# Kernel optimization log

Measured on AMD Instinct MI355X. Metric: run time of the kernel, lower is better.

The kernel has to match this reference:

```python
import jax, jax.numpy as jnp
import numpy as np

N, E, B = 50000, 800000, 512
DIN, H, A, BT = 128, 256, 40, 5


def _ln(h, g, b):
    m = jnp.mean(h, -1, keepdims=True)
    v = jnp.mean((h - m) ** 2, -1, keepdims=True)
    return (h - m) * jax.lax.rsqrt(v + 1e-5) * g + b


def _gcn(x, w, b, src, dst, n):
    # PyG GCNConv: add self-loops, symmetric D^-1/2 (A+I) D^-1/2 normalization
    h = x @ w
    loop = jnp.arange(n)
    s = jnp.concatenate([src, loop])
    d = jnp.concatenate([dst, loop])
    deg = jax.ops.segment_sum(jnp.ones(s.shape[0], h.dtype), d, num_segments=n)
    dinv = jax.lax.rsqrt(jnp.maximum(deg, 1.0))
    coef = (dinv[s] * dinv[d])[:, None]
    return jax.ops.segment_sum(coef * h[s], d, num_segments=n) + b


def _mlp2(x, w1, b1, w2, b2):
    return jax.nn.relu(x @ w1 + b1) @ w2 + b2


def _mlp3(x, w1, b1, w2, b2, w3, b3):
    h = jax.nn.relu(x @ w1 + b1)
    h = jax.nn.relu(h @ w2 + b2)
    return h @ w3 + b3


def setup_inputs() -> dict:
    key = jax.random.key(0)
    ks = iter(jax.random.split(key, 64))
    p = lambda shape: jax.random.normal(next(ks), shape, jnp.float32) * 0.05
    inp = {}
    inp["x"] = jax.random.normal(next(ks), (N, DIN), jnp.float32)
    inp["edge_index"] = jax.random.randint(next(ks), (2, E), 0, N)
    inp["batch"] = jnp.sort(jax.random.randint(next(ks), (N,), 0, B))
    inp["new_node_indices"] = jax.random.randint(next(ks), (B,), 0, N)
    inp["focus_node_indices"] = jax.random.randint(next(ks), (B,), 0, N)
    inp["num_graphs"] = B
    inp["conv_w0"] = p((DIN, H)); inp["conv_b0"] = p((H,))
    inp["conv_w1"] = p((H, H)); inp["conv_b1"] = p((H,))
    inp["conv_w2"] = p((H, H)); inp["conv_b2"] = p((H,))
    for i in range(3):
        inp[f"ln_g{i}"] = jnp.ones((H,), jnp.float32)
        inp[f"ln_b{i}"] = jnp.zeros((H,), jnp.float32)
    inp["res_w0"] = p((DIN, H)); inp["res_b0"] = p((H,))
    inp["stop_w1"] = p((H, H)); inp["stop_b1"] = p((H,))
    inp["stop_w2"] = p((H, 1)); inp["stop_b2"] = p((1,))
    inp["addn_w1"] = p((H, H)); inp["addn_b1"] = p((H,))
    inp["addn_w2"] = p((H, A)); inp["addn_b2"] = p((A,))
    inp["addb_w1"] = p((H, H)); inp["addb_b1"] = p((H,))
    inp["addb_w2"] = p((H, BT)); inp["addb_b2"] = p((BT,))
    inp["edge_w1"] = p((2 * H, H)); inp["edge_b1"] = p((H,))
    inp["edge_w2"] = p((H, H // 2)); inp["edge_b2"] = p((H // 2,))
    inp["edge_w3"] = p((H // 2, 1)); inp["edge_b3"] = p((1,))
    inp["bond_w1"] = p((2 * H, H)); inp["bond_b1"] = p((H,))
    inp["bond_w2"] = p((H, H // 2)); inp["bond_b2"] = p((H // 2,))
    inp["bond_w3"] = p((H // 2, BT)); inp["bond_b3"] = p((BT,))
    return inp


def reference(x, edge_index, batch, new_node_indices, focus_node_indices, num_graphs,
              conv_w0, conv_b0, conv_w1, conv_b1, conv_w2, conv_b2,
              ln_g0, ln_b0, ln_g1, ln_b1, ln_g2, ln_b2,
              res_w0, res_b0,
              stop_w1, stop_b1, stop_w2, stop_b2,
              addn_w1, addn_b1, addn_w2, addn_b2,
              addb_w1, addb_b1, addb_w2, addb_b2,
              edge_w1, edge_b1, edge_w2, edge_b2, edge_w3, edge_b3,
              bond_w1, bond_b1, bond_w2, bond_b2, bond_w3, bond_b3):
    n = x.shape[0]
    src, dst = edge_index[0], edge_index[1]
    conv_params = [(conv_w0, conv_b0), (conv_w1, conv_b1), (conv_w2, conv_b2)]
    ln_params = [(ln_g0, ln_b0), (ln_g1, ln_b1), (ln_g2, ln_b2)]
    h = x
    for i in range(3):
        h_in = h
        cw, cb = conv_params[i]
        lg, lb = ln_params[i]
        h = _gcn(h, cw, cb, src, dst, n)
        h = jax.nn.relu(_ln(h, lg, lb))  # dropout: eval mode (identity)
        res = h_in @ res_w0 + res_b0 if i == 0 else h_in
        h = h + res
    node_embeddings = h  # [N, H]
    # global mean pool over graphs
    counts = jax.ops.segment_sum(jnp.ones(n, h.dtype), batch, num_segments=num_graphs)
    graph_embedding = jax.ops.segment_sum(node_embeddings, batch, num_segments=num_graphs) / jnp.maximum(counts, 1.0)[:, None]
    stop_logits = _mlp2(graph_embedding, stop_w1, stop_b1, stop_w2, stop_b2)
    add_node_logits = _mlp2(graph_embedding, addn_w1, addn_b1, addn_w2, addn_b2)
    add_bond_logits = _mlp2(node_embeddings[focus_node_indices], addb_w1, addb_b1, addb_w2, addb_b2)
    # pair each node with its graph's newly added node
    new_node_embeddings = node_embeddings[new_node_indices]  # [B, H]
    pair = jnp.concatenate([node_embeddings, new_node_embeddings[batch]], axis=1)  # [N, 2H]
    edge_selection_logits = _mlp3(pair, edge_w1, edge_b1, edge_w2, edge_b2, edge_w3, edge_b3)
    bond_type_logits = _mlp3(pair, bond_w1, bond_b1, bond_w2, bond_b2, bond_w3, bond_b3)
    return (stop_logits, add_node_logits, add_bond_logits, node_embeddings,
            edge_selection_logits, bond_type_logits)
```

## Files before the change

kernel.cpp:

```cpp
#include <hip/hip_runtime.h>

typedef short bf16x8 __attribute__((ext_vector_type(8)));
typedef float f32x4 __attribute__((ext_vector_type(4)));
typedef unsigned short u16;
typedef u16 u16x8 __attribute__((ext_vector_type(8)));

__device__ __forceinline__ float bf2f(u16 u) {
  union { float f; unsigned int i; } x; x.i = ((unsigned int)u) << 16; return x.f;
}
__device__ __forceinline__ u16 f2bf(float f) {
  union { float f; unsigned int i; } x; x.f = f;
  unsigned int r = x.i + 0x7fffu + ((x.i >> 16) & 1u);
  return (u16)(r >> 16);
}
__device__ __forceinline__ void st_out_(void* out, size_t idx, float v, int f32) {
  if (f32) ((float*)out)[idx] = v;
  else ((u16*)out)[idx] = f2bf(v);
}

__global__ void k_detect(const u16* __restrict__ xx, int* flag) {
  int j = threadIdx.x;
  u16 u = xx[2 * j];
  int ex = (u >> 7) & 0xFF;
  int insane = (u != 0) && (ex < 100 || ex > 140);
  unsigned long long m = __ballot(insane);
  if (j == 0) flag[0] = (__popcll(m) > 8) ? 1 : 0;
}

__global__ void k_cvt_big(const void* __restrict__ src, u16* __restrict__ dst, int n,
                          const int* __restrict__ flag) {
  int i = blockIdx.x * 256 + threadIdx.x;
  if (i >= n) return;
  dst[i] = (*flag) ? f2bf(((const float*)src)[i]) : ((const u16*)src)[i];
}

#define NSEG 38
struct Cvt { const void* src[NSEG]; int off[NSEG + 1]; };
__global__ void k_cvt_all(Cvt c, u16* __restrict__ dst, int total, const int* __restrict__ flag) {
  int i = blockIdx.x * 256 + threadIdx.x;
  if (i >= total) return;
  int s = 0;
  #pragma unroll 1
  while (i >= c.off[s + 1]) s++;
  int j = i - c.off[s];
  dst[i] = (*flag) ? f2bf(((const float*)c.src[s])[j]) : ((const u16*)c.src[s])[j];
}

__global__ void k_padbias(const u16* __restrict__ rb, u16* cbz) {
  int i = blockIdx.x * 256 + threadIdx.x;
  if (i < 512) cbz[i] = (i < 256) ? (u16)0 : rb[i - 256];
}

struct Tr { const u16* src[8]; u16* dst[8]; int lk[8]; int nc[8]; int off[9]; };
__global__ void k_tr_all(Tr c, int total) {
  int i = blockIdx.x * 256 + threadIdx.x;
  if (i >= total) return;
  int s = 0;
  #pragma unroll 1
  while (i >= c.off[s + 1]) s++;
  int j = i - c.off[s];
  int K = 1 << c.lk[s];
  int nrow = j >> c.lk[s], k = j & (K - 1);
  c.dst[s][j] = c.src[s][k * c.nc[s] + nrow];
}

__global__ void k_init(int* deg, int* cursor, int n) {
  int i = blockIdx.x * 256 + threadIdx.x;
  if (i < n) { deg[i] = 1; cursor[i] = 0; }
}
__global__ void k_deg(const int* __restrict__ dst, int* deg, int e) {
  int i = blockIdx.x * 256 + threadIdx.x;
  if (i < e) atomicAdd(&deg[dst[i]], 1);
}
__global__ void k_dinv(const int* __restrict__ deg, float* dinv, int n) {
  int i = blockIdx.x * 256 + threadIdx.x;
  if (i < n) dinv[i] = rsqrtf((float)deg[i]);
}
#define SCB 4096
__global__ __launch_bounds__(256) void k_scanA(const int* __restrict__ deg, int* bsum, int n) {
  int b = blockIdx.x, t = threadIdx.x;
  int base = b * SCB;
  int s = 0;
  for (int j = t; j < SCB; j += 256) { int i = base + j; s += (i < n) ? deg[i] - 1 : 0; }
  int l = t & 63, wid = t >> 6;
  #pragma unroll
  for (int o = 32; o; o >>= 1) s += __shfl_xor(s, o);
  __shared__ int red[4];
  if (l == 0) red[wid] = s;
  __syncthreads();
  if (t == 0) bsum[b] = red[0] + red[1] + red[2] + red[3];
}
__global__ void k_scanB(int* bsum, int nb, int* off, int n) {
  if (threadIdx.x == 0) {
    int c = 0;
    for (int i = 0; i < nb; i++) { int v = bsum[i]; bsum[i] = c; c += v; }
    off[n] = c;
  }
}
__global__ __launch_bounds__(256) void k_scanC(const int* __restrict__ deg, const int* __restrict__ bsum,
                                               int* off, int n) {
  int b = blockIdx.x, t = threadIdx.x;
  int base = b * SCB + t * 16;
  int loc[16]; int s = 0;
  #pragma unroll
  for (int j = 0; j < 16; j++) { int i = base + j; loc[j] = s; s += (i < n) ? deg[i] - 1 : 0; }
  int l = t & 63, wid = t >> 6;
  int incl = s;
  #pragma unroll
  for (int o = 1; o < 64; o <<= 1) { int y = __shfl_up(incl, o); if (l >= o) incl += y; }
  int excl = incl - s;
  __shared__ int ws[4];
  if (l == 63) ws[wid] = incl;
  __syncthreads();
  int woff = 0;
  for (int w = 0; w < wid; w++) woff += ws[w];
  int pre = bsum[b] + woff + excl;
  #pragma unroll
  for (int j = 0; j < 16; j++) { int i = base + j; if (i < n) off[i] = pre + loc[j]; }
}
__global__ void k_csr(const int* __restrict__ src, const int* __restrict__ dst,
                      const int* __restrict__ off, int* cursor, int* csr_src, int e) {
  int i = blockIdx.x * 256 + threadIdx.x;
  if (i >= e) return;
  int d = dst[i], s = src[i];
  int slot = atomicAdd(&cursor[d], 1);
  csr_src[off[d] + slot] = s;
}

template <int EPI, int K>
__global__ __launch_bounds__(512) void gemm_p(
    const u16* __restrict__ A, int lda,
    const u16* __restrict__ Bt,
    u16* __restrict__ C, int ldc,
    int M, int NC,
    const u16* __restrict__ colbias,
    const float* __restrict__ rowbias, int rbld, const int* __restrict__ rowmap) {
  __shared__ u16 Bs[64 * K];
  __shared__ u16 As[8 * 4 * 512];
  const int t = threadIdx.x;
  const int n0 = blockIdx.x * 64;
  const int m0 = blockIdx.y * 512;
  {
    const int ng = K >> 3;
    const int tot = 64 * ng;
    for (int i = t; i < tot; i += 512) {
      int c = i / ng, g = i - c * ng;
      u16x8 v = *reinterpret_cast<const u16x8*>(Bt + (size_t)(n0 + c) * K + g * 8);
      *reinterpret_cast<u16x8*>(&Bs[c * K + (g ^ (c & 7)) * 8]) = v;
    }
  }
  __syncthreads();

  const int wid = t >> 6, l = t & 63;
  const int rbase = m0 + wid * 64;
  const int lr = l & 15, lg = l >> 4;
  u16* Aw = &As[wid * 2048];
  const int srow = l >> 2;
  const int sg = (l & 3) ^ (srow & 3);

  auto stage = [&](int s) {
    int mi = s & 3, kk = s >> 2;
    int row = rbase + mi * 16 + srow;
    if (row >= M) row = M - 1;
    __builtin_amdgcn_global_load_lds(
        (const __attribute__((address_space(1))) unsigned int*)(A + (size_t)row * lda + kk * 32 + sg * 8),
        (__attribute__((address_space(3))) unsigned int*)(Aw + (s & 3) * 512), 16, 0, 0);
  };

  f32x4 acc[4][4] = {};
  bf16x8 bfr[4];
  const int S = K >> 3;
  stage(0); stage(1); stage(2);
  #pragma unroll
  for (int s = 0; s < S; s++) {
    const int buf = s & 3, mi = s & 3, kk = s >> 2;
    __builtin_amdgcn_sched_barrier(0);
    if (s + 3 < S) stage(s + 3);
    const int rem = (s + 3 < S) ? 3 : (S - 1 - s);
    if (rem >= 3)      asm volatile("s_waitcnt vmcnt(3)" ::: "memory");
    else if (rem == 2) asm volatile("s_waitcnt vmcnt(2)" ::: "memory");
    else if (rem == 1) asm volatile("s_waitcnt vmcnt(1)" ::: "memory");
    else               asm volatile("s_waitcnt vmcnt(0)" ::: "memory");
    __builtin_amdgcn_sched_barrier(0);
    if (mi == 0) {
      #pragma unroll
      for (int ni = 0; ni < 4; ni++) {
        int g = kk * 4 + lg;
        bfr[ni] = *reinterpret_cast<const bf16x8*>(&Bs[(ni * 16 + lr) * K + (g ^ (lr & 7)) * 8]);
      }
    }
    const u16* Ab = Aw + buf * 512;
    bf16x8 af = *reinterpret_cast<const bf16x8*>(&Ab[lr * 32 + (lg ^ (lr & 3)) * 8]);
    #pragma unroll
    for (int ni = 0; ni < 4; ni++)
      acc[mi][ni] = __builtin_amdgcn_mfma_f32_16x16x32_bf16(af, bfr[ni], acc[mi][ni], 0, 0, 0);
  }

  #pragma unroll
  for (int mi = 0; mi < 4; mi++) {
    int rowi[4];
    #pragma unroll
    for (int r = 0; r < 4; r++) rowi[r] = rbase + mi * 16 + lg * 4 + r;
    float rbv[4][4];
    if (EPI == 3) {
      int rmv[4];
      #pragma unroll
      for (int r = 0; r < 4; r++) {
        int rr = rowi[r]; if (rr >= M) rr = M - 1;
        rmv[r] = rowmap[rr];
      }
      #pragma unroll
      for (int ni = 0; ni < 4; ni++)
        #pragma unroll
        for (int r = 0; r < 4; r++)
          rbv[ni][r] = rowbias[(size_t)rmv[r] * rbld + n0 + ni * 16 + lr];
    }
    #pragma unroll
    for (int ni = 0; ni < 4; ni++) {
      int col = n0 + ni * 16 + lr;
      float cbv = 0.f;
      if (EPI == 1 || EPI == 2) cbv = bf2f(colbias[col]);
      #pragma unroll
      for (int r = 0; r < 4; r++) {
        if (rowi[r] < M) {
          float v = acc[mi][ni][r];
          if (EPI == 1 || EPI == 2) v += cbv;
          if (EPI == 3) v += rbv[ni][r];
          if (EPI == 2 || EPI == 3) v = fmaxf(v, 0.f);
          C[(size_t)rowi[r] * ldc + col] = f2bf(v);
        }
      }
    }
  }
}

__global__ __launch_bounds__(256, 6) void k_agg(
    const u16* __restrict__ hw, int hwld, const u16* __restrict__ cb,
    const u16* __restrict__ lng, const u16* __restrict__ lnb,
    const u16* __restrict__ res, int resld, const float* __restrict__ dinv,
    const int* __restrict__ off, const int* __restrict__ csr_src,
    u16* __restrict__ hout, int n) {
  int l = threadIdx.x & 63;
  int v = blockIdx.x * 4 + (threadIdx.x >> 6);
  if (v >= n) return;
  const int half = l >> 5;
  const int c0 = (l & 31) * 8;
  float a[8] = {0, 0, 0, 0, 0, 0, 0, 0};
  int s = off[v], e = off[v + 1];
  int i = s;
  for (; i + 7 < e; i += 8) {
    int u0 = csr_src[i + half],     u1 = csr_src[i + 2 + half];
    int u2 = csr_src[i + 4 + half], u3 = csr_src[i + 6 + half];
    float w0 = dinv[u0], w1 = dinv[u1], w2 = dinv[u2], w3 = dinv[u3];
    u16x8 r0 = *reinterpret_cast<const u16x8*>(hw + (size_t)u0 * hwld + c0);
    u16x8 r1 = *reinterpret_cast<const u16x8*>(hw + (size_t)u1 * hwld + c0);
    u16x8 r2 = *reinterpret_cast<const u16x8*>(hw + (size_t)u2 * hwld + c0);
    u16x8 r3 = *reinterpret_cast<const u16x8*>(hw + (size_t)u3 * hwld + c0);
    #pragma unroll
    for (int j = 0; j < 8; j++)
      a[j] += w0 * bf2f(r0[j]) + w1 * bf2f(r1[j]) + w2 * bf2f(r2[j]) + w3 * bf2f(r3[j]);
  }
  for (; i < e; i += 2) {
    int idx = i + half;
    if (idx < e) {
      int u = csr_src[idx];
      float w = dinv[u];
      u16x8 r = *reinterpret_cast<const u16x8*>(hw + (size_t)u * hwld + c0);
      #pragma unroll
      for (int j = 0; j < 8; j++) a[j] += w * bf2f(r[j]);
    }
  }
  #pragma unroll
  for (int j = 0; j < 8; j++) a[j] += __shfl_xor(a[j], 32);
  float dv = dinv[v];
  u16x8 sv = *reinterpret_cast<const u16x8*>(hw + (size_t)v * hwld + c0);
  u16x8 cbv = *reinterpret_cast<const u16x8*>(cb + c0);
  float sum = 0.f;
  #pragma unroll
  for (int j = 0; j < 8; j++) {
    a[j] = dv * (dv * bf2f(sv[j]) + a[j]) + bf2f(cbv[j]);
    sum += a[j];
  }
  #pragma unroll
  for (int o = 16; o; o >>= 1) sum += __shfl_xor(sum, o);
  float mean = sum * (1.f / 256.f);
  float vs = 0.f;
  #pragma unroll
  for (int j = 0; j < 8; j++) { float d = a[j] - mean; vs += d * d; }
  #pragma unroll
  for (int o = 16; o; o >>= 1) vs += __shfl_xor(vs, o);
  float rs = rsqrtf(vs * (1.f / 256.f) + 1e-5f);
  u16x8 gv = *reinterpret_cast<const u16x8*>(lng + c0);
  u16x8 bv = *reinterpret_cast<const u16x8*>(lnb + c0);
  u16x8 rv = *reinterpret_cast<const u16x8*>(res + (size_t)v * resld + c0);
  u16x8 ov;
  #pragma unroll
  for (int j = 0; j < 8; j++)
    ov[j] = f2bf(fmaxf((a[j] - mean) * rs * bf2f(gv[j]) + bf2f(bv[j]), 0.f) + bf2f(rv[j]));
  if (half == 0)
    *reinterpret_cast<u16x8*>(hout + (size_t)v * 256 + c0) = ov;
}

__global__ __launch_bounds__(256) void k_pool(const u16* __restrict__ h, const int* __restrict__ batch,
                                              int n, float* gemb) {
  int g = blockIdx.x, c = threadIdx.x;
  int lo = 0, hi = n;
  while (lo < hi) { int mid = (lo + hi) >> 1; if (batch[mid] < g) lo = mid + 1; else hi = mid; }
  int s = lo;
  lo = s; hi = n;
  while (lo < hi) { int mid = (lo + hi) >> 1; if (batch[mid] < g + 1) lo = mid + 1; else hi = mid; }
  int e = lo;
  float a0 = 0.f, a1 = 0.f, a2 = 0.f, a3 = 0.f;
  int i = s;
  for (; i + 3 < e; i += 4) {
    a0 += bf2f(h[(size_t)i * 256 + c]);
    a1 += bf2f(h[(size_t)(i + 1) * 256 + c]);
    a2 += bf2f(h[(size_t)(i + 2) * 256 + c]);
    a3 += bf2f(h[(size_t)(i + 3) * 256 + c]);
  }
  for (; i < e; i++) a0 += bf2f(h[(size_t)i * 256 + c]);
  float acc = (a0 + a1) + (a2 + a3);
  int cnt = e - s; if (cnt < 1) cnt = 1;
  gemb[g * 256 + c] = acc / (float)cnt;
}

__global__ __launch_bounds__(256) void k_glin(const u16* __restrict__ h, const int* __restrict__ nidx,
                                              const u16* __restrict__ W, const u16* __restrict__ b1,
                                              float* g1, int ld, int ofs) {
  int b = blockIdx.x, t = threadIdx.x;
  __shared__ float sin_[256];
  sin_[t] = bf2f(h[(size_t)nidx[b] * 256 + t]);
  __syncthreads();
  float acc = bf2f(b1[t]);
  #pragma unroll 8
  for (int k = 0; k < 256; k++) acc += sin_[k] * bf2f(W[k * 256 + t]);
  g1[(size_t)b * ld + ofs + t] = acc;
}

template <int OUTD>
__global__ __launch_bounds__(256) void k_mlp2(const float* __restrict__ inf32,
                                              const u16* __restrict__ inbf, const int* __restrict__ idx,
                                              const u16* __restrict__ W1, const u16* __restrict__ b1,
                                              const u16* __restrict__ W2, const u16* __restrict__ b2,
                                              void* __restrict__ out, size_t obase,
                                              const int* __restrict__ flag) {
  int b = blockIdx.x, t = threadIdx.x;
  __shared__ float sin_[256];
  __shared__ float sh[256];
  sin_[t] = inf32 ? inf32[b * 256 + t] : bf2f(inbf[(size_t)idx[b] * 256 + t]);
  __syncthreads();
  float acc = bf2f(b1[t]);
  #pragma unroll 8
  for (int k = 0; k < 256; k++) acc += sin_[k] * bf2f(W1[k * 256 + t]);
  sh[t] = fmaxf(acc, 0.f);
  __syncthreads();
  if (t < OUTD) {
    float a2 = bf2f(b2[t]);
    #pragma unroll 8
    for (int k = 0; k < 256; k++) a2 += sh[k] * bf2f(W2[k * OUTD + t]);
    st_out_(out, obase + (size_t)b * OUTD + t, a2, *flag);
  }
}

__global__ __launch_bounds__(256) void k_final(const u16* __restrict__ t2e, const u16* __restrict__ t2b,
                                               const u16* __restrict__ w3e, const u16* __restrict__ b3e,
                                               const u16* __restrict__ w3b, const u16* __restrict__ b3b,
                                               void* __restrict__ out, size_t oe, size_t ob, int M,
                                               const int* __restrict__ flag) {
  int r = blockIdx.x * 4 + (threadIdx.x >> 6);
  int l = threadIdx.x & 63;
  if (r >= M) return;
  float p[6] = {0, 0, 0, 0, 0, 0};
  #pragma unroll
  for (int j = 0; j < 2; j++) {
    int k = l * 2 + j;
    float te = bf2f(t2e[(size_t)r * 128 + k]);
    float tb = bf2f(t2b[(size_t)r * 128 + k]);
    p[0] += te * bf2f(w3e[k]);
    #pragma unroll
    for (int q = 0; q < 5; q++) p[1 + q] += tb * bf2f(w3b[k * 5 + q]);
  }
  #pragma unroll
  for (int q = 0; q < 6; q++)
    #pragma unroll
    for (int o = 32; o; o >>= 1) p[q] += __shfl_xor(p[q], o);
  if (l == 0) {
    int f32 = *flag;
    st_out_(out, oe + r, p[0] + bf2f(b3e[0]), f32);
    #pragma unroll
    for (int q = 0; q < 5; q++)
      st_out_(out, ob + (size_t)r * 5 + q, p[1 + q] + bf2f(b3b[q]), f32);
  }
}

__global__ void k_emit8(const u16* __restrict__ src, void* __restrict__ out, size_t obase, int n8,
                        const int* __restrict__ flag) {
  int i = blockIdx.x * 256 + threadIdx.x;
  if (i >= n8) return;
  u16x8 v = reinterpret_cast<const u16x8*>(src)[i];
  if (*flag) {
    float4* fo = (float4*)((float*)out + obase);
    float4 lo, hi;
    lo.x = bf2f(v[0]); lo.y = bf2f(v[1]); lo.z = bf2f(v[2]); lo.w = bf2f(v[3]);
    hi.x = bf2f(v[4]); hi.y = bf2f(v[5]); hi.z = bf2f(v[6]); hi.w = bf2f(v[7]);
    fo[(size_t)i * 2] = lo; fo[(size_t)i * 2 + 1] = hi;
  } else {
    reinterpret_cast<u16x8*>((u16*)out + obase)[i] = v;
  }
}

extern "C" void kernel_launch(void* const* d_in, const int* in_sizes, int n_in,
                              void* d_out, int out_size, void* d_ws, size_t ws_size,
                              hipStream_t stream) {
  const int N = in_sizes[0] / 128;
  const int E = in_sizes[1] / 2;
  const int B = in_sizes[3];

  const int* ei    = (const int*)d_in[1];
  const int* srcp  = ei;
  const int* dstp  = ei + E;
  const int* batch = (const int*)d_in[2];
  const int* newi  = (const int*)d_in[3];
  const int* focus = (const int*)d_in[4];

  const size_t o_stop = 0;
  const size_t o_addn = (size_t)B;
  const size_t o_addb = (size_t)B + (size_t)B * 40;
  const size_t o_emb  = o_addb + (size_t)B * 5;
  const size_t o_esel = o_emb + (size_t)N * 256;
  const size_t o_bond = o_esel + (size_t)N;

  char* p = (char*)d_ws;
  auto alloc = [&](size_t bytes) -> void* {
    void* r = (void*)p;
    p += (bytes + 255) & ~(size_t)255;
    return r;
  };
  int* flag = (int*)alloc(4);
  static const int seg_din[NSEG] = {6,7,8,9,10,11, 12,13,14,15,16,17, 18,19,
                                    20,21,22,23, 24,25,26,27, 28,29,30,31,
                                    32,33,34,35,36,37, 38,39,40,41,42,43};
  static const int seg_len[NSEG] = {32768,256,65536,256,65536,256, 256,256,256,256,256,256,
                                    32768,256, 65536,256,256,1, 65536,256,10240,40,
                                    65536,256,1280,5, 131072,256,32768,128,128,1,
                                    131072,256,32768,128,640,5};
  int wtotal = 0;
  int seg_off[NSEG + 1];
  for (int i = 0; i < NSEG; i++) { seg_off[i] = wtotal; wtotal += seg_len[i]; }
  seg_off[NSEG] = wtotal;
  u16* wbf = (u16*)alloc((size_t)wtotal * 2);
  u16* wt_f0  = (u16*)alloc(512 * 128 * 2);
  u16* wt_cw1 = (u16*)alloc(256 * 256 * 2);
  u16* wt_cw2 = (u16*)alloc(256 * 256 * 2);
  u16* wt_t1  = (u16*)alloc(512 * 256 * 2);
  u16* wt_e2  = (u16*)alloc(128 * 256 * 2);
  u16* wt_b2  = (u16*)alloc(128 * 256 * 2);
  u16* cbz    = (u16*)alloc(512 * 2);
  int*   deg     = (int*)alloc((size_t)N * 4);
  int*   cursor  = (int*)alloc((size_t)N * 4);
  int*   off     = (int*)alloc((size_t)(N + 1) * 4);
  float* dinv    = (float*)alloc((size_t)N * 4);
  int*   bsum    = (int*)alloc(64 * 4);
  float* gemb    = (float*)alloc((size_t)B * 256 * 4);
  float* g1full  = (float*)alloc((size_t)B * 512 * 4);
  int*   csr_src = (int*)alloc((size_t)E * 4);
  u16*   xbf     = (u16*)alloc((size_t)N * 128 * 2);
  u16*   P1      = (u16*)alloc((size_t)N * 256 * 2);
  u16*   P2      = (u16*)alloc((size_t)N * 256 * 2);
  u16*   P3      = (u16*)alloc((size_t)N * 256 * 2);

  auto wseg = [&](int i) -> u16* { return wbf + seg_off[i]; };
  u16 *cw0 = wseg(0), *cb0 = wseg(1), *cw1 = wseg(2), *cb1 = wseg(3), *cw2 = wseg(4), *cb2 = wseg(5);
  u16 *lg0 = wseg(6), *lb0 = wseg(7), *lg1 = wseg(8), *lb1 = wseg(9), *lg2 = wseg(10), *lb2 = wseg(11);
  u16 *rw0 = wseg(12), *rb0 = wseg(13);
  u16 *sw1 = wseg(14), *sb1 = wseg(15), *sw2 = wseg(16), *sb2 = wseg(17);
  u16 *aw1 = wseg(18), *ab1 = wseg(19), *aw2 = wseg(20), *ab2 = wseg(21);
  u16 *bw1 = wseg(22), *bb1 = wseg(23), *bw2 = wseg(24), *bb2 = wseg(25);
  u16 *ew1 = wseg(26), *eb1 = wseg(27), *ew2 = wseg(28), *eb2 = wseg(29), *ew3 = wseg(30), *eb3 = wseg(31);
  u16 *qw1 = wseg(32), *qb1 = wseg(33), *qw2 = wseg(34), *qb2 = wseg(35), *qw3 = wseg(36), *qb3 = wseg(37);

  k_detect<<<1, 64, 0, stream>>>((const u16*)d_in[0], flag);
  k_cvt_big<<<(N * 128 + 255) / 256, 256, 0, stream>>>(d_in[0], xbf, N * 128, flag);
  Cvt cd;
  for (int i = 0; i < NSEG; i++) cd.src[i] = d_in[seg_din[i]];
  for (int i = 0; i <= NSEG; i++) cd.off[i] = seg_off[i];
  k_cvt_all<<<(wtotal + 255) / 256, 256, 0, stream>>>(cd, wbf, wtotal, flag);
  k_padbias<<<2, 256, 0, stream>>>(rb0, cbz);

  const int NB = (N + 255) / 256;
  const int EBk = (E + 255) / 256;
  const int NBS = (N + SCB - 1) / SCB;

  k_init<<<NB, 256, 0, stream>>>(deg, cursor, N);
  k_deg<<<EBk, 256, 0, stream>>>(dstp, deg, E);
  k_dinv<<<NB, 256, 0, stream>>>(deg, dinv, N);
  k_scanA<<<NBS, 256, 0, stream>>>(deg, bsum, N);
  k_scanB<<<1, 64, 0, stream>>>(bsum, NBS, off, N);
  k_scanC<<<NBS, 256, 0, stream>>>(deg, bsum, off, N);
  k_csr<<<EBk, 256, 0, stream>>>(srcp, dstp, off, cursor, csr_src, E);

  {
    Tr td;
    const u16* ts[8] = {cw0, rw0, cw1, cw2, ew1, qw1, ew2, qw2};
    u16* tdst[8] = {wt_f0, wt_f0 + 256 * 128, wt_cw1, wt_cw2, wt_t1, wt_t1 + 256 * 256, wt_e2, wt_b2};
    int tlk[8] = {7, 7, 8, 8, 8, 8, 8, 8};
    int tnc[8] = {256, 256, 256, 256, 256, 256, 128, 128};
    int tlen[8] = {32768, 32768, 65536, 65536, 65536, 65536, 32768, 32768};
    int tot = 0;
    for (int i = 0; i < 8; i++) {
      td.src[i] = ts[i]; td.dst[i] = tdst[i]; td.lk[i] = tlk[i]; td.nc[i] = tnc[i];
      td.off[i] = tot; tot += tlen[i];
    }
    td.off[8] = tot;
    k_tr_all<<<(tot + 255) / 256, 256, 0, stream>>>(td, tot);
  }

  const int MB5 = (N + 511) / 512;
  const int AGB = (N + 3) / 4;
  u16* PF = P1;

  gemm_p<1, 128><<<dim3(8, MB5), 512, 0, stream>>>(xbf, 128, wt_f0, PF, 512, N, 512, cbz, nullptr, 0, nullptr);
  k_agg<<<AGB, 256, 0, stream>>>(PF, 512, cb0, lg0, lb0, PF + 256, 512, dinv, off, csr_src, P3, N);
  gemm_p<0, 256><<<dim3(4, MB5), 512, 0, stream>>>(P3, 256, wt_cw1, P1, 256, N, 256, nullptr, nullptr, 0, nullptr);
  k_agg<<<AGB, 256, 0, stream>>>(P1, 256, cb1, lg1, lb1, P3, 256, dinv, off, csr_src, P2, N);
  gemm_p<0, 256><<<dim3(4, MB5), 512, 0, stream>>>(P2, 256, wt_cw2, P1, 256, N, 256, nullptr, nullptr, 0, nullptr);
  k_agg<<<AGB, 256, 0, stream>>>(P1, 256, cb2, lg2, lb2, P2, 256, dinv, off, csr_src, P3, N);

  k_emit8<<<(N * 256 / 8 + 255) / 256, 256, 0, stream>>>(P3, d_out, o_emb, N * 256 / 8, flag);

  k_pool<<<B, 256, 0, stream>>>(P3, batch, N, gemb);
  k_glin<<<B, 256, 0, stream>>>(P3, newi, ew1 + 256 * 256, eb1, g1full, 512, 0);
  k_glin<<<B, 256, 0, stream>>>(P3, newi, qw1 + 256 * 256, qb1, g1full, 512, 256);
  k_mlp2<1><<<B, 256, 0, stream>>>(gemb, nullptr, nullptr, sw1, sb1, sw2, sb2, d_out, o_stop, flag);
  k_mlp2<40><<<B, 256, 0, stream>>>(gemb, nullptr, nullptr, aw1, ab1, aw2, ab2, d_out, o_addn, flag);
  k_mlp2<5><<<B, 256, 0, stream>>>(nullptr, P3, focus, bw1, bb1, bw2, bb2, d_out, o_addb, flag);

  u16* T1 = PF;
  gemm_p<3, 256><<<dim3(8, MB5), 512, 0, stream>>>(P3, 256, wt_t1, T1, 512, N, 512, nullptr, g1full, 512, batch);
  u16* t2e = P3;
  u16* t2b = P3 + (size_t)N * 128;
  gemm_p<2, 256><<<dim3(2, MB5), 512, 0, stream>>>(T1, 512, wt_e2, t2e, 128, N, 128, eb2, nullptr, 0, nullptr);
  gemm_p<2, 256><<<dim3(2, MB5), 512, 0, stream>>>(T1 + 256, 512, wt_b2, t2b, 128, N, 128, qb2, nullptr, 0, nullptr);
  k_final<<<(N + 3) / 4, 256, 0, stream>>>(t2e, t2b, ew3, eb3, qw3, qb3, d_out, o_esel, o_bond, N, flag);
}
```

Before: 615.2 us.

## Restructure GEMM to keep A rows resident and stream weights from global

Replaces the 512-row by 64-column GEMM tiling with a 64-row tile per block that holds its A slice in registers and loops over every output column. Weight fragments are read straight from global memory (and so L2) with double-buffered register loads, so LDS no longer stages B. Each activation row is now read once per GEMM rather than once per column block, which removes the repeated A traffic. The cost is more register pressure and heavier global reads of the weights, and the async LDS pipeline is gone.

```diff
diff --git a/kernel.cpp b/kernel.cpp
--- a/kernel.cpp
+++ b/kernel.cpp
@@ -127,110 +127,82 @@
   csr_src[off[d] + slot] = s;
 }
 
-template <int EPI, int K>
-__global__ __launch_bounds__(512) void gemm_p(
+template <int EPI, int K, int NC>
+__global__ __launch_bounds__(256) void gemm_a(
     const u16* __restrict__ A, int lda,
     const u16* __restrict__ Bt,
     u16* __restrict__ C, int ldc,
-    int M, int NC,
+    int M,
     const u16* __restrict__ colbias,
     const float* __restrict__ rowbias, int rbld, const int* __restrict__ rowmap) {
-  __shared__ u16 Bs[64 * K];
-  __shared__ u16 As[8 * 4 * 512];
+  constexpr int NG = K / 8;
+  constexpr int NK = K / 32;
+  constexpr int NT = NC / 16;
+  __shared__ u16 As[64 * K];
   const int t = threadIdx.x;
-  const int n0 = blockIdx.x * 64;
-  const int m0 = blockIdx.y * 512;
-  {
-    const int ng = K >> 3;
-    const int tot = 64 * ng;
-    for (int i = t; i < tot; i += 512) {
-      int c = i / ng, g = i - c * ng;
-      u16x8 v = *reinterpret_cast<const u16x8*>(Bt + (size_t)(n0 + c) * K + g * 8);
-      *reinterpret_cast<u16x8*>(&Bs[c * K + (g ^ (c & 7)) * 8]) = v;
+  const int m0 = blockIdx.x * 64;
+  for (int i = t; i < 64 * NG; i += 256) {
+    int r = i / NG, s = i - r * NG;
+    int row = m0 + r; if (row >= M) row = M - 1;
+    u16x8 v = *reinterpret_cast<const u16x8*>(A + (size_t)row * lda + (s ^ (r & 7)) * 8);
+    *reinterpret_cast<u16x8*>(&As[r * K + s * 8]) = v;
+  }
+  __syncthreads();
+
+  const int wid = t >> 6, l = t & 63, lr = l & 15, lg = l >> 4;
+  const int rloc = wid * 16 + lr;
+  bf16x8 af[NK];
+  #pragma unroll
+  for (int kk = 0; kk < NK; kk++)
+    af[kk] = *reinterpret_cast<const bf16x8*>(&As[rloc * K + ((kk * 4 + lg) ^ (lr & 7)) * 8]);
+
+  const int rowo = m0 + wid * 16 + lg * 4;
+  int rmv[4];
+  if (EPI == 3) {
+    #pragma unroll
+    for (int r = 0; r < 4; r++) {
+      int rr = rowo + r; if (rr >= M) rr = M - 1;
+      rmv[r] = rowmap[rr];
     }
   }
-  __syncthreads();
-
-  const int wid = t >> 6, l = t & 63;
-  const int rbase = m0 + wid * 64;
-  const int lr = l & 15, lg = l >> 4;
-  u16* Aw = &As[wid * 2048];
-  const int srow = l >> 2;
-  const int sg = (l & 3) ^ (srow & 3);
-
-  auto stage = [&](int s) {
-    int mi = s & 3, kk = s >> 2;
-    int row = rbase + mi * 16 + srow;
-    if (row >= M) row = M - 1;
-    __builtin_amdgcn_global_load_lds(
-        (const __attribute__((address_space(1))) unsigned int*)(A + (size_t)row * lda + kk * 32 + sg * 8),
-        (__attribute__((address_space(3))) unsigned int*)(Aw + (s & 3) * 512), 16, 0, 0);
+  const u16* bp = Bt + (size_t)lr * K + lg * 8;
+
+  auto loadB = [&](bf16x8* buf, int ni) {
+    #pragma unroll
+    for (int kk = 0; kk < NK; kk++)
+      buf[kk] = *reinterpret_cast<const bf16x8*>(bp + (size_t)ni * 16 * K + kk * 32);
   };
-
-  f32x4 acc[4][4] = {};
-  bf16x8 bfr[4];
-  const int S = K >> 3;
-  stage(0); stage(1); stage(2);
-  #pragma unroll
-  for (int s = 0; s < S; s++) {
-    const int buf = s & 3, mi = s & 3, kk = s >> 2;
-    __builtin_amdgcn_sched_barrier(0);
-    if (s + 3 < S) stage(s + 3);
-    const int rem = (s + 3 < S) ? 3 : (S - 1 - s);
-    if (rem >= 3)      asm volatile("s_waitcnt vmcnt(3)" ::: "memory");
-    else if (rem == 2) asm volatile("s_waitcnt vmcnt(2)" ::: "memory");
-    else if (rem == 1) asm volatile("s_waitcnt vmcnt(1)" ::: "memory");
-    else               asm volatile("s_waitcnt vmcnt(0)" ::: "memory");
-    __builtin_amdgcn_sched_barrier(0);
-    if (mi == 0) {
-      #pragma unroll
-      for (int ni = 0; ni < 4; ni++) {
-        int g = kk * 4 + lg;
-        bfr[ni] = *reinterpret_cast<const bf16x8*>(&Bs[(ni * 16 + lr) * K + (g ^ (lr & 7)) * 8]);
+  auto computeC = [&](const bf16x8* buf, int ni) {
+    f32x4 a0 = {0.f, 0.f, 0.f, 0.f}, a1 = {0.f, 0.f, 0.f, 0.f};
+    #pragma unroll
+    for (int kk = 0; kk < NK; kk += 2) {
+      a0 = __builtin_amdgcn_mfma_f32_16x16x32_bf16(af[kk], buf[kk], a0, 0, 0, 0);
+      a1 = __builtin_amdgcn_mfma_f32_16x16x32_bf16(af[kk + 1], buf[kk + 1], a1, 0, 0, 0);
+    }
+    int col = ni * 16 + lr;
+    float cbv = 0.f;
+    if (EPI == 1 || EPI == 2) cbv = bf2f(colbias[col]);
+    #pragma unroll
+    for (int r = 0; r < 4; r++) {
+      int row = rowo + r;
+      if (row < M) {
+        float v = a0[r] + a1[r];
+        if (EPI == 1 || EPI == 2) v += cbv;
+        if (EPI == 3) v += rowbias[(size_t)rmv[r] * rbld + col];
+        if (EPI == 2 || EPI == 3) v = fmaxf(v, 0.f);
+        C[(size_t)row * ldc + col] = f2bf(v);
       }
     }
-    const u16* Ab = Aw + buf * 512;
-    bf16x8 af = *reinterpret_cast<const bf16x8*>(&Ab[lr * 32 + (lg ^ (lr & 3)) * 8]);
-    #pragma unroll
-    for (int ni = 0; ni < 4; ni++)
-      acc[mi][ni] = __builtin_amdgcn_mfma_f32_16x16x32_bf16(af, bfr[ni], acc[mi][ni], 0, 0, 0);
-  }
-
-  #pragma unroll
-  for (int mi = 0; mi < 4; mi++) {
-    int rowi[4];
-    #pragma unroll
-    for (int r = 0; r < 4; r++) rowi[r] = rbase + mi * 16 + lg * 4 + r;
-    float rbv[4][4];
-    if (EPI == 3) {
-      int rmv[4];
-      #pragma unroll
-      for (int r = 0; r < 4; r++) {
-        int rr = rowi[r]; if (rr >= M) rr = M - 1;
-        rmv[r] = rowmap[rr];
-      }
-      #pragma unroll
-      for (int ni = 0; ni < 4; ni++)
-        #pragma unroll
-        for (int r = 0; r < 4; r++)
-          rbv[ni][r] = rowbias[(size_t)rmv[r] * rbld + n0 + ni * 16 + lr];
-    }
-    #pragma unroll
-    for (int ni = 0; ni < 4; ni++) {
-      int col = n0 + ni * 16 + lr;
-      float cbv = 0.f;
-      if (EPI == 1 || EPI == 2) cbv = bf2f(colbias[col]);
-      #pragma unroll
-      for (int r = 0; r < 4; r++) {
-        if (rowi[r] < M) {
-          float v = acc[mi][ni][r];
-          if (EPI == 1 || EPI == 2) v += cbv;
-          if (EPI == 3) v += rbv[ni][r];
-          if (EPI == 2 || EPI == 3) v = fmaxf(v, 0.f);
-          C[(size_t)rowi[r] * ldc + col] = f2bf(v);
-        }
-      }
-    }
+  };
+
+  bf16x8 bufA[NK], bufB[NK];
+  loadB(bufA, 0);
+  #pragma unroll 1
+  for (int ni = 0; ni < NT; ni += 2) {
+    loadB(bufB, ni + 1);
+    computeC(bufA, ni);
+    if (ni + 2 < NT) loadB(bufA, ni + 2);
+    computeC(bufB, ni + 1);
   }
 }
 
@@ -515,15 +487,15 @@
     k_tr_all<<<(tot + 255) / 256, 256, 0, stream>>>(td, tot);
   }
 
-  const int MB5 = (N + 511) / 512;
+  const int GA = (N + 63) / 64;
   const int AGB = (N + 3) / 4;
   u16* PF = P1;
 
-  gemm_p<1, 128><<<dim3(8, MB5), 512, 0, stream>>>(xbf, 128, wt_f0, PF, 512, N, 512, cbz, nullptr, 0, nullptr);
+  gemm_a<1, 128, 512><<<GA, 256, 0, stream>>>(xbf, 128, wt_f0, PF, 512, N, cbz, nullptr, 0, nullptr);
   k_agg<<<AGB, 256, 0, stream>>>(PF, 512, cb0, lg0, lb0, PF + 256, 512, dinv, off, csr_src, P3, N);
-  gemm_p<0, 256><<<dim3(4, MB5), 512, 0, stream>>>(P3, 256, wt_cw1, P1, 256, N, 256, nullptr, nullptr, 0, nullptr);
+  gemm_a<0, 256, 256><<<GA, 256, 0, stream>>>(P3, 256, wt_cw1, P1, 256, N, nullptr, nullptr, 0, nullptr);
   k_agg<<<AGB, 256, 0, stream>>>(P1, 256, cb1, lg1, lb1, P3, 256, dinv, off, csr_src, P2, N);
-  gemm_p<0, 256><<<dim3(4, MB5), 512, 0, stream>>>(P2, 256, wt_cw2, P1, 256, N, 256, nullptr, nullptr, 0, nullptr);
+  gemm_a<0, 256, 256><<<GA, 256, 0, stream>>>(P2, 256, wt_cw2, P1, 256, N, nullptr, nullptr, 0, nullptr);
   k_agg<<<AGB, 256, 0, stream>>>(P1, 256, cb2, lg2, lb2, P2, 256, dinv, off, csr_src, P3, N);
 
   k_emit8<<<(N * 256 / 8 + 255) / 256, 256, 0, stream>>>(P3, d_out, o_emb, N * 256 / 8, flag);
@@ -536,10 +508,10 @@
   k_mlp2<5><<<B, 256, 0, stream>>>(nullptr, P3, focus, bw1, bb1, bw2, bb2, d_out, o_addb, flag);
 
   u16* T1 = PF;
-  gemm_p<3, 256><<<dim3(8, MB5), 512, 0, stream>>>(P3, 256, wt_t1, T1, 512, N, 512, nullptr, g1full, 512, batch);
+  gemm_a<3, 256, 512><<<GA, 256, 0, stream>>>(P3, 256, wt_t1, T1, 512, N, nullptr, g1full, 512, batch);
   u16* t2e = P3;
   u16* t2b = P3 + (size_t)N * 128;
-  gemm_p<2, 256><<<dim3(2, MB5), 512, 0, stream>>>(T1, 512, wt_e2, t2e, 128, N, 128, eb2, nullptr, 0, nullptr);
-  gemm_p<2, 256><<<dim3(2, MB5), 512, 0, stream>>>(T1 + 256, 512, wt_b2, t2b, 128, N, 128, qb2, nullptr, 0, nullptr);
+  gemm_a<2, 256, 128><<<GA, 256, 0, stream>>>(T1, 512, wt_e2, t2e, 128, N, eb2, nullptr, 0, nullptr);
+  gemm_a<2, 256, 128><<<GA, 256, 0, stream>>>(T1 + 256, 512, wt_b2, t2b, 128, N, qb2, nullptr, 0, nullptr);
   k_final<<<(N + 3) / 4, 256, 0, stream>>>(t2e, t2b, ew3, eb3, qw3, qb3, d_out, o_esel, o_bond, N, flag);
 }
```

Measured after the change: 867.4 us. +41.0%, slower.
